# Kernel tuning notes

Measured on AMD Instinct MI355X. Metric: run time of the kernel, lower is better.

The kernel has to match this reference:

```python
import jax, jax.numpy as jnp
import numpy as np

B, T_STEPS, H, W = 8192, 512, 64, 64


def setup_inputs() -> dict:
    key = jax.random.key(0)
    k_w, k_g, k_i, k_j, k_a = jax.random.split(key, 5)
    walls = (jax.random.uniform(k_w, (B, H, W)) < 0.3).astype(jnp.float32)
    walls = walls.at[:, 0, :].set(1.0).at[:, H - 1, :].set(1.0)
    walls = walls.at[:, :, 0].set(1.0).at[:, :, W - 1].set(1.0)
    # goals: sparse cells with value 10 (the code checks goals[...] == 10)
    goals = jnp.where(jax.random.uniform(k_g, (B, H, W)) < 0.02, 10.0, 0.0).astype(jnp.float32)
    # start positions strictly interior; clear the wall at each start cell
    i0 = jax.random.randint(k_i, (B,), 1, H - 1)
    j0 = jax.random.randint(k_j, (B,), 1, W - 1)
    walls = walls.at[jnp.arange(B), i0, j0].set(0.0)
    world = jnp.stack([walls, goals], axis=1)  # [B, 2, H, W]
    s0 = jnp.stack([i0, j0], axis=1).astype(jnp.float32)  # [B, 2]
    a = jax.random.randint(k_a, (B, T_STEPS), 0, 5).astype(jnp.int32)  # actions in {0..4}
    return {"s0": s0, "a": a, "world": world, "T": T_STEPS}


def _rollout(s0, a, world, T):
    walls = world[:, 0].reshape(world.shape[0], -1)  # [B, H*W]
    goals = world[:, 1].reshape(world.shape[0], -1)  # [B, H*W]
    Wd = world.shape[3]

    def step(s, a_t):
        # action deltas: 1 -> row-1, 2 -> row+1, 3 -> col-1, 4 -> col+1, 0 -> stay
        dr = jnp.where(a_t == 1, -1.0, jnp.where(a_t == 2, 1.0, 0.0))
        dc = jnp.where(a_t == 3, -1.0, jnp.where(a_t == 4, 1.0, 0.0))
        s_new = s + jnp.stack([dr, dc], axis=1).astype(s.dtype)  # [B, 2]
        idx = (s_new[:, 0].astype(jnp.int32) * Wd + s_new[:, 1].astype(jnp.int32))[:, None]
        g = jnp.take_along_axis(goals, idx, axis=1)[:, 0]
        w = jnp.take_along_axis(walls, idx, axis=1)[:, 0]
        hit_goal = g == 10.0
        hit_wall = jnp.logical_and(jnp.logical_not(hit_goal), w == 1.0)
        r = jnp.where(hit_goal, 1.0, jnp.where(hit_wall, -1.0, -0.01)).astype(jnp.float32)
        s_next = jnp.where(hit_wall[:, None], s, s_new)  # revert move on wall hit
        return s_next, (s_next, r)

    _, (s_traj, r_traj) = jax.lax.scan(step, s0, jnp.swapaxes(a[:, :T], 0, 1))
    s_full = jnp.concatenate([s0[:, None, :], jnp.swapaxes(s_traj, 0, 1)], axis=1)  # [B, T+1, 2]
    r0 = jnp.zeros((s0.shape[0], 1), dtype=jnp.float32)
    r_full = jnp.concatenate([r0, jnp.swapaxes(r_traj, 0, 1)], axis=1)  # [B, T+1]
    return s_full, r_full


def reference(s0, a, world, T):
    return _rollout(s0, a, world, T)
```

## Files before the change

### kernel.cpp

```cpp
#include <hip/hip_runtime.h>
#include <stdint.h>

#define T_STEPS 512
#define CELLS   4096
#define BPB     16
#define THREADS 64

__device__ __forceinline__ uint32_t pack4(float4 w, float4 g) {
    uint32_t b0 = (g.x == 10.0f) ? 2u : ((w.x == 1.0f) ? 1u : 0u);
    uint32_t b1 = (g.y == 10.0f) ? 2u : ((w.y == 1.0f) ? 1u : 0u);
    uint32_t b2 = (g.z == 10.0f) ? 2u : ((w.z == 1.0f) ? 1u : 0u);
    uint32_t b3 = (g.w == 10.0f) ? 2u : ((w.w == 1.0f) ? 1u : 0u);
    return b0 | (b1 << 8) | (b2 << 16) | (b3 << 24);
}

__global__ __launch_bounds__(THREADS) void rollout_kernel(
    const float* __restrict__ s0,
    const int*   __restrict__ act,
    const float* __restrict__ world,
    float* __restrict__ out,
    int B)
{
    __shared__ uint8_t cells[BPB * CELLS];

    const int tid = threadIdx.x;
    const int b0  = blockIdx.x * BPB;

    for (int bb = 0; bb < BPB; ++bb) {
        const float* wbase = world + (size_t)(b0 + bb) * (2 * CELLS);
        const float* gbase = wbase + CELLS;
        #pragma unroll
        for (int h = 0; h < 4; ++h) {
            const int c0 = h * 1024 + tid * 16;
            float4 w0 = *(const float4*)(wbase + c0);
            float4 w1 = *(const float4*)(wbase + c0 + 4);
            float4 w2 = *(const float4*)(wbase + c0 + 8);
            float4 w3 = *(const float4*)(wbase + c0 + 12);
            float4 g0 = *(const float4*)(gbase + c0);
            float4 g1 = *(const float4*)(gbase + c0 + 4);
            float4 g2 = *(const float4*)(gbase + c0 + 8);
            float4 g3 = *(const float4*)(gbase + c0 + 12);
            uint4 v = make_uint4(pack4(w0, g0), pack4(w1, g1),
                                 pack4(w2, g2), pack4(w3, g3));
            *(uint4*)(&cells[bb * CELLS + c0]) = v;
        }
    }
    __syncthreads();

    if (tid < BPB) {
        const int b = b0 + tid;
        float2 s = *(const float2*)(s0 + 2 * (size_t)b);
        int r = (int)s.x;
        int c = (int)s.y;
        int p = r * 64 + c;
        const uint8_t* my = cells + tid * CELLS;

        float* s_out = out + (size_t)b * (2 * (T_STEPS + 1));
        float* r_out = out + (size_t)B * (2 * (T_STEPS + 1)) + (size_t)b * (T_STEPS + 1);

        *(float2*)s_out = s;
        r_out[0] = 0.0f;

        const int4* ap = (const int4*)(act + (size_t)b * T_STEPS);
        int4 cur = ap[0];
        for (int k = 0; k < T_STEPS / 4; ++k) {
            int4 nxt = (k + 1 < T_STEPS / 4) ? ap[k + 1] : cur;
            int as4[4] = {cur.x, cur.y, cur.z, cur.w};
            #pragma unroll
            for (int j = 0; j < 4; ++j) {
                const int t = k * 4 + j;
                const int a = as4[j];
                const int dr = (a == 1) ? -1 : ((a == 2) ? 1 : 0);
                const int dc = (a == 3) ? -1 : ((a == 4) ? 1 : 0);
                const int p1 = p + dr * 64 + dc;
                const int idxn = p1 + ((p1 < 0) ? CELLS : 0);
                const int cell = ((unsigned)idxn < (unsigned)CELLS) ? my[idxn] : 0;
                const bool hw = (cell == 1);
                const float rew = (cell == 2) ? 1.0f : (hw ? -1.0f : -0.01f);
                const int r1 = r + dr, c1 = c + dc;
                if (!hw) { r = r1; c = c1; p = p1; }
                float2 sv = make_float2((float)r, (float)c);
                *(float2*)(s_out + 2 * (t + 1)) = sv;
                r_out[t + 1] = rew;
            }
            cur = nxt;
        }
    }
}

extern "C" void kernel_launch(void* const* d_in, const int* in_sizes, int n_in,
                              void* d_out, int out_size, void* d_ws, size_t ws_size,
                              hipStream_t stream) {
    const float* s0    = (const float*)d_in[0];
    const int*   act   = (const int*)d_in[1];
    const float* world = (const float*)d_in[2];
    float*       out   = (float*)d_out;

    const int B = in_sizes[0] / 2;
    const int grid = B / BPB;

    rollout_kernel<<<grid, THREADS, 0, stream>>>(s0, act, world, out, B);
}
```

Before: 469.9 us.

## Speculate two steps per lookup round, deepen action prefetch, shrink batches per block

Each pair of steps now issues three shared-memory lookups at once (the first move plus both outcomes of the second move) and picks the result with selects. This shortens the serial lookup-dependency chain across steps at the cost of an extra LDS read per pair. Action loads are prefetched three int4s ahead instead of one, and BPB drops from 16 to 4. The smaller BPB cuts the shared-memory tile and quadruples the block count, which should raise occupancy and latency hiding, but leaves only 4 active lanes per wave.

```diff
diff --git a/kernel.cpp b/kernel.cpp
--- a/kernel.cpp
+++ b/kernel.cpp
@@ -3,7 +3,7 @@
 
 #define T_STEPS 512
 #define CELLS   4096
-#define BPB     16
+#define BPB     4
 #define THREADS 64
 
 __device__ __forceinline__ uint32_t pack4(float4 w, float4 g) {
@@ -26,6 +26,7 @@
     const int tid = threadIdx.x;
     const int b0  = blockIdx.x * BPB;
 
+    #pragma unroll
     for (int bb = 0; bb < BPB; ++bb) {
         const float* wbase = world + (size_t)(b0 + bb) * (2 * CELLS);
         const float* gbase = wbase + CELLS;
@@ -55,6 +56,12 @@
         int p = r * 64 + c;
         const uint8_t* my = cells + tid * CELLS;
 
+        auto lookup = [&](int q) -> int {
+            const int idx = q + ((q < 0) ? CELLS : 0);
+            const int cell = my[idx & (CELLS - 1)];
+            return ((unsigned)idx < (unsigned)CELLS) ? cell : 0;
+        };
+
         float* s_out = out + (size_t)b * (2 * (T_STEPS + 1));
         float* r_out = out + (size_t)B * (2 * (T_STEPS + 1)) + (size_t)b * (T_STEPS + 1);
 
@@ -62,28 +69,46 @@
         r_out[0] = 0.0f;
 
         const int4* ap = (const int4*)(act + (size_t)b * T_STEPS);
-        int4 cur = ap[0];
+        int4 A0 = ap[0];
+        int4 A1 = ap[1];
+        int4 A2 = ap[2];
         for (int k = 0; k < T_STEPS / 4; ++k) {
-            int4 nxt = (k + 1 < T_STEPS / 4) ? ap[k + 1] : cur;
-            int as4[4] = {cur.x, cur.y, cur.z, cur.w};
+            const int4 A3 = (k + 3 < T_STEPS / 4) ? ap[k + 3] : A0;
+            const int as4[4] = {A0.x, A0.y, A0.z, A0.w};
             #pragma unroll
-            for (int j = 0; j < 4; ++j) {
-                const int t = k * 4 + j;
-                const int a = as4[j];
-                const int dr = (a == 1) ? -1 : ((a == 2) ? 1 : 0);
-                const int dc = (a == 3) ? -1 : ((a == 4) ? 1 : 0);
-                const int p1 = p + dr * 64 + dc;
-                const int idxn = p1 + ((p1 < 0) ? CELLS : 0);
-                const int cell = ((unsigned)idxn < (unsigned)CELLS) ? my[idxn] : 0;
-                const bool hw = (cell == 1);
-                const float rew = (cell == 2) ? 1.0f : (hw ? -1.0f : -0.01f);
-                const int r1 = r + dr, c1 = c + dc;
-                if (!hw) { r = r1; c = c1; p = p1; }
-                float2 sv = make_float2((float)r, (float)c);
-                *(float2*)(s_out + 2 * (t + 1)) = sv;
-                r_out[t + 1] = rew;
+            for (int jj = 0; jj < 2; ++jj) {
+                const int t  = k * 4 + jj * 2;
+                const int a0 = as4[2 * jj];
+                const int a1 = as4[2 * jj + 1];
+                const int d0r = (a0 == 1) ? -1 : ((a0 == 2) ? 1 : 0);
+                const int d0c = (a0 == 3) ? -1 : ((a0 == 4) ? 1 : 0);
+                const int d1r = (a1 == 1) ? -1 : ((a1 == 2) ? 1 : 0);
+                const int d1c = (a1 == 3) ? -1 : ((a1 == 4) ? 1 : 0);
+                const int e0 = d0r * 64 + d0c;
+                const int e1 = d1r * 64 + d1c;
+                const int q0  = p + e0;
+                const int q10 = p + e1;
+                const int q11 = q0 + e1;
+                const int l0  = lookup(q0);
+                const int l10 = lookup(q10);
+                const int l11 = lookup(q11);
+                const bool hw0  = (l0 == 1);
+                const float rew0 = (l0 == 2) ? 1.0f : (hw0 ? -1.0f : -0.01f);
+                const int p0  = hw0 ? p : q0;
+                const int r0v = hw0 ? r : r + d0r;
+                const int c0v = hw0 ? c : c + d0c;
+                const int l1 = hw0 ? l10 : l11;
+                const bool hw1  = (l1 == 1);
+                const float rew1 = (l1 == 2) ? 1.0f : (hw1 ? -1.0f : -0.01f);
+                p = hw1 ? p0 : p0 + e1;
+                r = hw1 ? r0v : r0v + d1r;
+                c = hw1 ? c0v : c0v + d1c;
+                *(float2*)(s_out + 2 * (t + 1)) = make_float2((float)r0v, (float)c0v);
+                *(float2*)(s_out + 2 * (t + 2)) = make_float2((float)r, (float)c);
+                r_out[t + 1] = rew0;
+                r_out[t + 2] = rew1;
             }
-            cur = nxt;
+            A0 = A1; A1 = A2; A2 = A3;
         }
     }
 }
```

Result: slower. 493.3 us (+5.0%).
